# Performance work log

Hardware: AMD Instinct MI355X
Metric: run time of the kernel (lower is better)

## Reference

```python
import jax, jax.numpy as jnp
import numpy as np

D_MODEL = 2048
D_STATE = 16
D_CONV = 4
EXPAND = 2
D_INNER = EXPAND * D_MODEL  # 4096
DT_RANK = 128               # ceil(2048/16)
BATCH = 2
SEQ = 1024


def setup_inputs() -> dict:
    key = jax.random.key(0)
    ks = jax.random.split(key, 10)
    n = lambda k, shape, scale: jax.random.normal(k, shape, dtype=jnp.float32) * scale
    # A_log = log(arange(1..N)) broadcast over channels, exactly as in the torch init
    A_log = jnp.log(jnp.tile(jnp.arange(1, D_STATE + 1, dtype=jnp.float32)[None, :], (D_INNER, 1)))
    return {
        "hidden_states": n(ks[0], (BATCH, SEQ, D_MODEL), 1.0),
        "W_in": n(ks[1], (2 * D_INNER, D_MODEL), 0.02),
        "conv_w": n(ks[2], (D_INNER, D_CONV), 0.2),
        "conv_b": n(ks[3], (D_INNER,), 0.02),
        "W_x": n(ks[4], (DT_RANK + 2 * D_STATE, D_INNER), 0.02),
        "W_dt": n(ks[5], (D_INNER, DT_RANK), 0.05),
        "b_dt": n(ks[6], (D_INNER,), 0.5) - 4.0,  # softplus(b_dt) ~ small dt, like inv-softplus init
        "A_log": A_log,
        "D_skip": jnp.ones((D_INNER,), jnp.float32),
        "W_out": n(ks[7], (D_MODEL, D_INNER), 0.02),
    }


def _mamba_forward(hidden_states, W_in, conv_w, conv_b, W_x, W_dt, b_dt, A_log, D_skip, W_out):
    B, L, _ = hidden_states.shape
    # in_proj then split into x (SSM path) and z (gate)
    xz = hidden_states @ W_in.T                      # (B, L, 2*Di)
    x, z = jnp.split(xz, 2, axis=-1)                 # (B, L, Di) each
    # causal depthwise conv1d (kernel D_CONV, left pad D_CONV-1) + SiLU
    xp = jnp.pad(x, ((0, 0), (D_CONV - 1, 0), (0, 0)))
    xc = conv_b
    for k in range(D_CONV):
        xc = xc + conv_w[:, k] * xp[:, k:k + L, :]
    x = jax.nn.silu(xc)                              # (B, L, Di)
    # input-dependent dt, B, C
    x_dbl = x @ W_x.T                                # (B, L, dt_rank + 2N)
    dt_low, B_in, C_in = jnp.split(x_dbl, [DT_RANK, DT_RANK + D_STATE], axis=-1)
    dt = dt_low @ W_dt.T                             # (B, L, Di); bias added inside scan (delta_bias)
    delta = jax.nn.softplus(dt + b_dt)               # (B, L, Di)
    A = -jnp.exp(A_log)                              # (Di, N)

    def step(h, inp):
        delta_t, u_t, B_t, C_t = inp                 # (B,Di),(B,Di),(B,N),(B,N)
        dA = jnp.exp(delta_t[..., None] * A)         # (B, Di, N)
        h = dA * h + (delta_t * u_t)[..., None] * B_t[:, None, :]
        y_t = jnp.einsum('bdn,bn->bd', h, C_t)
        return h, y_t

    h0 = jnp.zeros((B, D_INNER, D_STATE), x.dtype)
    xs = (jnp.swapaxes(delta, 0, 1), jnp.swapaxes(x, 0, 1),
          jnp.swapaxes(B_in, 0, 1), jnp.swapaxes(C_in, 0, 1))
    _, ys = jax.lax.scan(step, h0, xs)               # ys: (L, B, Di)
    y = jnp.swapaxes(ys, 0, 1)                       # (B, L, Di)
    y = y + D_skip * x                               # skip connection
    y = y * jax.nn.silu(z)                           # output gating
    return y @ W_out.T                               # (B, L, D_MODEL)


def reference(hidden_states, W_in, conv_w, conv_b, W_x, W_dt, b_dt, A_log, D_skip, W_out):
    return _mamba_forward(hidden_states, W_in, conv_w, conv_b, W_x, W_dt, b_dt, A_log, D_skip, W_out)
```

## Files before the change

### kernel.cpp

```cpp
#include <hip/hip_runtime.h>
#include <hip/hip_bf16.h>


#define BATCH 2
#define SEQ 1024
#define DMODEL 2048
#define DINNER 4096
#define DSTATE 16
#define DTRANK 128
#define ROWS (BATCH * SEQ)
#define XDBL_N (DTRANK + 2 * DSTATE)
#define NCHUNK 32
#define LOG2_NCHUNK 5
#define CLEN (SEQ / NCHUNK)
#define WXPAD 192
#define SPLITK 16

typedef unsigned short ushort_t;
typedef __attribute__((ext_vector_type(8))) short short8;
typedef __attribute__((ext_vector_type(4))) float f32x4;

__device__ __forceinline__ ushort_t bf16_rne(float f) {
  unsigned u = __float_as_uint(f);
  return (ushort_t)((u + 0x7FFFu + ((u >> 16) & 1u)) >> 16);
}

__global__ __launch_bounds__(256) void cast_bf16(
    const float* __restrict__ x, ushort_t* __restrict__ o, int n4) {
  int i = blockIdx.x * 256 + threadIdx.x;
  if (i >= n4) return;
  float4 v = ((const float4*)x)[i];
  ushort4 h;
  h.x = bf16_rne(v.x); h.y = bf16_rne(v.y);
  h.z = bf16_rne(v.z); h.w = bf16_rne(v.w);
  ((ushort4*)o)[i] = h;
}

__global__ __launch_bounds__(256) void cast_wx(
    const float* __restrict__ wx, ushort_t* __restrict__ o) {
  int i = blockIdx.x * 256 + threadIdx.x;
  if (i >= WXPAD * (DINNER / 4)) return;
  int row = i >> 10;
  ushort4 h = {0, 0, 0, 0};
  if (row < XDBL_N) {
    float4 v = ((const float4*)wx)[i];
    h.x = bf16_rne(v.x); h.y = bf16_rne(v.y);
    h.z = bf16_rne(v.z); h.w = bf16_rne(v.w);
  }
  ((ushort4*)o)[i] = h;
}

template <int TM, int TN, int EPI, bool SK, bool SWZ>
__global__ __launch_bounds__(256, 2) void gemm_bf16(
    const ushort_t* __restrict__ X, int lda,
    const ushort_t* __restrict__ W, int ldb,
    const float* __restrict__ bias,
    float* __restrict__ C, int ldc, int kslice, size_t sstride) {
  constexpr int MI = TM / 32;
  constexpr int NI = TN / 32;
  constexpr int G = (TM + TN) / 32;
  __shared__ __attribute__((aligned(16))) ushort_t lds[(TM + TN) * 64];

  const int tid = threadIdx.x;
  const int lane = tid & 63;
  const int w = tid >> 6;
  const int wm = w & 1, wn = w >> 1;
  int bx = blockIdx.x, by = blockIdx.y;
  if (SWZ) {
    const int bid = by * 16 + bx;
    const int cpx = (16 * gridDim.y) >> 3;
    const int sz = (bid & 7) * cpx + (bid >> 3);
    bx = sz & 15;
    by = sz >> 4;
  }
  const int m0 = bx * TM;
  const int n0 = by * TN;
  const int kbase = SK ? blockIdx.z * kslice : 0;

  const int lrow = lane >> 3;
  const int csw = (lane & 7) ^ lrow;
  const int quad = lane >> 4;
  const int l15 = lane & 15;
  const int x0 = quad ^ (lane & 7);
  const int baseA = (wm * (TM / 2) + l15) * 64;
  const int baseB = (TM + wn * (TN / 2) + l15) * 64;

  f32x4 acc[MI][NI] = {};

  for (int kt = 0; kt < kslice; kt += 64) {
#pragma unroll
    for (int j = 0; j < G; j++) {
      const int r0 = (w * G + j) * 8;
      const int row = r0 + lrow;
      const ushort_t* src = (r0 < TM)
          ? X + (size_t)(m0 + row) * lda + kbase + kt + csw * 8
          : W + (size_t)(n0 + row - TM) * ldb + kbase + kt + csw * 8;
      __builtin_amdgcn_global_load_lds(
          (const __attribute__((address_space(1))) unsigned int*)src,
          (__attribute__((address_space(3))) unsigned int*)&lds[r0 * 64],
          16, 0, 0);
    }
    __syncthreads();

#pragma unroll
    for (int ks = 0; ks < 2; ks++) {
      const int xo = (x0 ^ (ks * 4)) * 8;
      short8 a[MI], b[NI];
#pragma unroll
      for (int mi = 0; mi < MI; mi++)
        a[mi] = *(const short8*)&lds[baseA + mi * 1024 + xo];
#pragma unroll
      for (int ni = 0; ni < NI; ni++)
        b[ni] = *(const short8*)&lds[baseB + ni * 1024 + xo];
#pragma unroll
      for (int mi = 0; mi < MI; mi++)
#pragma unroll
        for (int ni = 0; ni < NI; ni++)
          acc[mi][ni] = __builtin_amdgcn_mfma_f32_16x16x32_bf16(
              a[mi], b[ni], acc[mi][ni], 0, 0, 0);
    }
    __syncthreads();
  }

  float* Cs = SK ? (C + (size_t)blockIdx.z * sstride) : C;
#pragma unroll
  for (int mi = 0; mi < MI; mi++)
#pragma unroll
    for (int ni = 0; ni < NI; ni++) {
      int row = m0 + wm * (TM / 2) + mi * 16 + quad * 4;
      int col = n0 + wn * (TN / 2) + ni * 16 + l15;
#pragma unroll
      for (int r = 0; r < 4; r++) {
        float v = acc[mi][ni][r];
        if (EPI == 1) {
          v += bias[col];
          v = (v > 20.f) ? v : log1pf(__expf(v));
        }
        Cs[(size_t)(row + r) * ldc + col] = v;
      }
    }
}

__device__ __forceinline__ void bar() {
  asm volatile("" ::: "memory");
  __builtin_amdgcn_s_barrier();
  asm volatile("" ::: "memory");
}
#define VMWAIT(n) asm volatile("s_waitcnt vmcnt(" #n ")" ::: "memory")
#define LGKM0 asm volatile("s_waitcnt lgkmcnt(0)" ::: "memory")
#define SCHED0 __builtin_amdgcn_sched_barrier(0)

#define CLUSTER(AF, BF, MH, NH)                                           \
  do {                                                                    \
    __builtin_amdgcn_s_setprio(1);                                        \
    _Pragma("unroll")                                                     \
    for (int mi = 0; mi < 4; mi++)                                        \
      _Pragma("unroll")                                                   \
      for (int ni = 0; ni < 2; ni++)                                      \
        _Pragma("unroll")                                                 \
        for (int ks = 0; ks < 2; ks++)                                    \
          acc[(MH) * 4 + mi][(NH) * 2 + ni] =                             \
              __builtin_amdgcn_mfma_f32_16x16x32_bf16(                    \
                  AF[mi][ks], BF[ni][ks],                                 \
                  acc[(MH) * 4 + mi][(NH) * 2 + ni], 0, 0, 0);            \
    __builtin_amdgcn_s_setprio(0);                                        \
  } while (0)

__global__ __launch_bounds__(512, 2) void gemm256(
    const ushort_t* __restrict__ X, int lda,
    const ushort_t* __restrict__ W, int ldb,
    float* __restrict__ C, int ldc, int K) {
  __shared__ __attribute__((aligned(16))) ushort_t lds[65536];
  const int tid = threadIdx.x;
  const int lane = tid & 63;
  const int w = tid >> 6;
  const int wm = w >> 2, wn = w & 3;
  const int bid = blockIdx.y * 8 + blockIdx.x;
  const int swz = (bid & 7) * 32 + (bid >> 3);
  const int m0 = (swz & 7) * 256;
  const int n0 = (swz >> 3) * 256;
  const int lrow = lane >> 3;
  const int csw = (lane & 7) ^ lrow;
  const int quad = lane >> 4;
  const int l15 = lane & 15;
  const int sx = lane & 7;

  f32x4 acc[8][4] = {};
  short8 a[4][2], b0[2][2], b1[2][2];

  const ushort_t* Asrc = X + (size_t)(m0 + w * 8 + lrow) * lda + csw * 8;
  const ushort_t* Bsrc = W + (size_t)(n0 + w * 8 + lrow) * ldb + csw * 8;

  auto stA = [&](int buf, int g, int kt) {
    __builtin_amdgcn_global_load_lds(
        (const __attribute__((address_space(1))) unsigned int*)
            (Asrc + (size_t)g * 64 * lda + kt),
        (__attribute__((address_space(3))) unsigned int*)
            &lds[buf * 16384 + (g * 64 + w * 8) * 64],
        16, 0, 0);
  };
  auto stB = [&](int buf, int g, int kt) {
    __builtin_amdgcn_global_load_lds(
        (const __attribute__((address_space(1))) unsigned int*)
            (Bsrc + (size_t)g * 64 * ldb + kt),
        (__attribute__((address_space(3))) unsigned int*)
            &lds[32768 + buf * 16384 + (g * 64 + w * 8) * 64],
        16, 0, 0);
  };
  auto rdA = [&](int buf, int half, int mi, int ks) {
    int row = wm * 128 + half * 64 + mi * 16 + l15;
    int ch = (ks * 4 + quad) ^ sx;
    return *(const short8*)&lds[buf * 16384 + row * 64 + ch * 8];
  };
  auto rdB = [&](int buf, int nh, int ni, int ks) {
    int row = wn * 64 + nh * 32 + ni * 16 + l15;
    int ch = (ks * 4 + quad) ^ sx;
    return *(const short8*)&lds[32768 + buf * 16384 + row * 64 + ch * 8];
  };

#pragma unroll
  for (int g = 0; g < 4; g++) stA(0, g, 0);
#pragma unroll
  for (int g = 0; g < 4; g++) stB(0, g, 0);
  VMWAIT(0);
  bar();

  const int NT = K / 64;
  int cur = 0;
  for (int t = 0; t < NT - 1; ++t) {
    const int nxt = cur ^ 1;
    const int k2 = (t + 1) * 64;
#pragma unroll
    for (int mi = 0; mi < 4; mi++)
#pragma unroll
      for (int ks = 0; ks < 2; ks++) a[mi][ks] = rdA(cur, 0, mi, ks);
#pragma unroll
    for (int ni = 0; ni < 2; ni++)
#pragma unroll
      for (int ks = 0; ks < 2; ks++) b0[ni][ks] = rdB(cur, 0, ni, ks);
    stB(nxt, 0, k2); stB(nxt, 1, k2); stA(nxt, 0, k2); stA(nxt, 2, k2);
    bar();
    LGKM0; SCHED0;
    CLUSTER(a, b0, 0, 0);
    bar();
#pragma unroll
    for (int ni = 0; ni < 2; ni++)
#pragma unroll
      for (int ks = 0; ks < 2; ks++) b1[ni][ks] = rdB(cur, 1, ni, ks);
    stB(nxt, 2, k2); stB(nxt, 3, k2); stA(nxt, 1, k2); stA(nxt, 3, k2);
    bar();
    LGKM0; SCHED0;
    CLUSTER(a, b1, 0, 1);
    VMWAIT(8);
    bar();
#pragma unroll
    for (int mi = 0; mi < 4; mi++)
#pragma unroll
      for (int ks = 0; ks < 2; ks++) a[mi][ks] = rdA(cur, 1, mi, ks);
    bar();
    LGKM0; SCHED0;
    CLUSTER(a, b1, 1, 1);
    bar();
    CLUSTER(a, b0, 1, 0);
    VMWAIT(2);
    bar();
    cur = nxt;
  }
  {
#pragma unroll
    for (int mi = 0; mi < 4; mi++)
#pragma unroll
      for (int ks = 0; ks < 2; ks++) a[mi][ks] = rdA(cur, 0, mi, ks);
#pragma unroll
    for (int ni = 0; ni < 2; ni++)
#pragma unroll
      for (int ks = 0; ks < 2; ks++) b0[ni][ks] = rdB(cur, 0, ni, ks);
    bar();
    LGKM0; SCHED0;
    CLUSTER(a, b0, 0, 0);
    bar();
#pragma unroll
    for (int ni = 0; ni < 2; ni++)
#pragma unroll
      for (int ks = 0; ks < 2; ks++) b1[ni][ks] = rdB(cur, 1, ni, ks);
    bar();
    LGKM0; SCHED0;
    CLUSTER(a, b1, 0, 1);
    VMWAIT(0);
    bar();
#pragma unroll
    for (int mi = 0; mi < 4; mi++)
#pragma unroll
      for (int ks = 0; ks < 2; ks++) a[mi][ks] = rdA(cur, 1, mi, ks);
    bar();
    LGKM0; SCHED0;
    CLUSTER(a, b1, 1, 1);
    CLUSTER(a, b0, 1, 0);
  }

#pragma unroll
  for (int mi = 0; mi < 8; mi++)
#pragma unroll
    for (int ni = 0; ni < 4; ni++) {
      int row = m0 + wm * 128 + mi * 16 + quad * 4;
      int col = n0 + wn * 64 + ni * 16 + l15;
#pragma unroll
      for (int r = 0; r < 4; r++)
        C[(size_t)(row + r) * ldc + col] = acc[mi][ni][r];
    }
}

__global__ __launch_bounds__(192) void reduce_sk(
    const float* __restrict__ partials, float* __restrict__ xdbl,
    ushort_t* __restrict__ dtb) {
  int m = blockIdx.x;
  int c = threadIdx.x;
  if (c >= XDBL_N) return;
  float s = 0.f;
#pragma unroll
  for (int z = 0; z < SPLITK; z++)
    s += partials[(size_t)z * ROWS * WXPAD + (size_t)m * WXPAD + c];
  xdbl[(size_t)m * XDBL_N + c] = s;
  if (c < DTRANK) dtb[(size_t)m * DTRANK + c] = bf16_rne(s);
}

__global__ __launch_bounds__(256) void conv_silu(
    const float* __restrict__ xz, const float* __restrict__ cw,
    const float* __restrict__ cb, float* __restrict__ xs,
    ushort_t* __restrict__ xsb) {
  int idx = blockIdx.x * 256 + threadIdx.x;
  if (idx >= ROWS * DINNER / 4) return;
  int d4 = idx & (DINNER / 4 - 1);
  int bt = idx >> 10;
  int t = bt & (SEQ - 1);
  int d = d4 * 4;
  float4 c4 = *(const float4*)&cb[d];
  float wv[4][4];
  *(float4*)wv[0] = *(const float4*)&cw[(d + 0) * 4];
  *(float4*)wv[1] = *(const float4*)&cw[(d + 1) * 4];
  *(float4*)wv[2] = *(const float4*)&cw[(d + 2) * 4];
  *(float4*)wv[3] = *(const float4*)&cw[(d + 3) * 4];
  float a0 = c4.x, a1 = c4.y, a2 = c4.z, a3 = c4.w;
#pragma unroll
  for (int k = 0; k < 4; k++) {
    int tt = t - 3 + k;
    if (tt >= 0) {
      float4 v = *(const float4*)&xz[(size_t)(bt - 3 + k) * (2 * DINNER) + d];
      a0 += wv[0][k] * v.x;
      a1 += wv[1][k] * v.y;
      a2 += wv[2][k] * v.z;
      a3 += wv[3][k] * v.w;
    }
  }
  float4 s;
  s.x = a0 / (1.f + __expf(-a0));
  s.y = a1 / (1.f + __expf(-a1));
  s.z = a2 / (1.f + __expf(-a2));
  s.w = a3 / (1.f + __expf(-a3));
  *(float4*)&xs[(size_t)bt * DINNER + d] = s;
  ushort4 h;
  h.x = bf16_rne(s.x); h.y = bf16_rne(s.y);
  h.z = bf16_rne(s.z); h.w = bf16_rne(s.w);
  *(ushort4*)&xsb[(size_t)bt * DINNER + d] = h;
}

__global__ __launch_bounds__(256) void scan_pass1(
    const float* __restrict__ delta, const float* __restrict__ xs,
    const float* __restrict__ xdbl, const float* __restrict__ A_log,
    float* __restrict__ hpart, float* __restrict__ sumd) {
  int g = blockIdx.x * 256 + threadIdx.x;
  int d = g & (DINNER - 1);
  int rest = g >> 12;
  int c = rest & (NCHUNK - 1);
  int b = rest >> LOG2_NCHUNK;

  float Adn[16];
#pragma unroll
  for (int q = 0; q < 4; q++) {
    float4 a = *(const float4*)&A_log[d * 16 + q * 4];
    Adn[q * 4 + 0] = -__expf(a.x); Adn[q * 4 + 1] = -__expf(a.y);
    Adn[q * 4 + 2] = -__expf(a.z); Adn[q * 4 + 3] = -__expf(a.w);
  }

  float h[16] = {};
  float sd = 0.f;
  const size_t t0 = (size_t)b * SEQ + c * CLEN;
  const float* dp = delta + t0 * DINNER + d;
  const float* up = xs + t0 * DINNER + d;
  const float* xb = xdbl + t0 * XDBL_N + DTRANK;

  for (int i = 0; i < CLEN; i++) {
    float dt = dp[(size_t)i * DINNER];
    float u = up[(size_t)i * DINNER];
    sd += dt;
    float du = dt * u;
    float Bv[16];
#pragma unroll
    for (int q = 0; q < 4; q++)
      *(float4*)&Bv[q * 4] = *(const float4*)&xb[i * XDBL_N + q * 4];
#pragma unroll
    for (int n = 0; n < 16; n++)
      h[n] = __expf(dt * Adn[n]) * h[n] + du * Bv[n];
  }

  float* hp = hpart + ((size_t)(c * BATCH + b) * DINNER + d) * 16;
#pragma unroll
  for (int q = 0; q < 4; q++) *(float4*)&hp[q * 4] = *(const float4*)&h[q * 4];
  sumd[(size_t)(c * BATCH + b) * DINNER + d] = sd;
}

__global__ __launch_bounds__(256) void scan_pass2(
    float* __restrict__ hph, const float* __restrict__ sumd,
    const float* __restrict__ A_log) {
  int g = blockIdx.x * 256 + threadIdx.x;
  int n = g & 15;
  int d = (g >> 4) & (DINNER - 1);
  int b = g >> 16;

  float Adn = -__expf(A_log[d * 16 + n]);
  float h = 0.f;
  for (int c = 0; c < NCHUNK; c++) {
    size_t base = (size_t)(c * BATCH + b) * DINNER + d;
    float part = hph[base * 16 + n];
    hph[base * 16 + n] = h;
    h = __expf(Adn * sumd[base]) * h + part;
  }
}

__global__ __launch_bounds__(256) void scan_pass3(
    const float* __restrict__ xz, const float* __restrict__ xs,
    const float* __restrict__ xdbl, const float* __restrict__ A_log,
    const float* __restrict__ D_skip, const float* __restrict__ h0,
    const float* __restrict__ delta, ushort_t* __restrict__ gated) {
  int g = blockIdx.x * 256 + threadIdx.x;
  int d = g & (DINNER - 1);
  int rest = g >> 12;
  int c = rest & (NCHUNK - 1);
  int b = rest >> LOG2_NCHUNK;

  float Adn[16];
#pragma unroll
  for (int q = 0; q < 4; q++) {
    float4 a = *(const float4*)&A_log[d * 16 + q * 4];
    Adn[q * 4 + 0] = -__expf(a.x); Adn[q * 4 + 1] = -__expf(a.y);
    Adn[q * 4 + 2] = -__expf(a.z); Adn[q * 4 + 3] = -__expf(a.w);
  }
  float Dd = D_skip[d];

  float h[16];
  const float* hp = h0 + ((size_t)(c * BATCH + b) * DINNER + d) * 16;
#pragma unroll
  for (int q = 0; q < 4; q++) *(float4*)&h[q * 4] = *(const float4*)&hp[q * 4];

  const size_t t0 = (size_t)b * SEQ + c * CLEN;
  const float* dl = delta + t0 * DINNER + d;
  const float* up = xs + t0 * DINNER + d;
  const float* zb = xz + t0 * (2 * DINNER) + DINNER + d;
  const float* xb = xdbl + t0 * XDBL_N + DTRANK;
  ushort_t* gp = gated + t0 * DINNER + d;

  for (int i = 0; i < CLEN; i++) {
    float dt = dl[(size_t)i * DINNER];
    float u = up[(size_t)i * DINNER];
    float du = dt * u;
    float Bv[16], Cv[16];
#pragma unroll
    for (int q = 0; q < 4; q++) {
      *(float4*)&Bv[q * 4] = *(const float4*)&xb[i * XDBL_N + q * 4];
      *(float4*)&Cv[q * 4] = *(const float4*)&xb[i * XDBL_N + DSTATE + q * 4];
    }
    float y = 0.f;
#pragma unroll
    for (int n = 0; n < 16; n++) {
      h[n] = __expf(dt * Adn[n]) * h[n] + du * Bv[n];
      y += h[n] * Cv[n];
    }
    float z = zb[(size_t)i * (2 * DINNER)];
    float sz = z / (1.f + __expf(-z));
    gp[(size_t)i * DINNER] = bf16_rne((y + Dd * u) * sz);
  }
}

extern "C" void kernel_launch(void* const* d_in, const int* in_sizes, int n_in,
                              void* d_out, int out_size, void* d_ws, size_t ws_size,
                              hipStream_t stream) {
  const float* hidden = (const float*)d_in[0];
  const float* W_in   = (const float*)d_in[1];
  const float* conv_w = (const float*)d_in[2];
  const float* conv_b = (const float*)d_in[3];
  const float* W_x    = (const float*)d_in[4];
  const float* W_dt   = (const float*)d_in[5];
  const float* b_dt   = (const float*)d_in[6];
  const float* A_log  = (const float*)d_in[7];
  const float* D_skip = (const float*)d_in[8];
  const float* W_out  = (const float*)d_in[9];
  float* out = (float*)d_out;

  float* ws    = (float*)d_ws;
  float* xz    = ws;
  float* xs    = xz + (size_t)ROWS * 2 * DINNER;
  float* xdbl  = xs + (size_t)ROWS * DINNER;
  float* delta = xdbl + (size_t)ROWS * XDBL_N;
  float* sumd  = delta + (size_t)ROWS * DINNER;
  float* hph   = sumd + (size_t)BATCH * DINNER * NCHUNK;
  ushort_t* Hb   = (ushort_t*)(hph + (size_t)BATCH * DINNER * NCHUNK * DSTATE);
  ushort_t* Wb1  = Hb + (size_t)ROWS * DMODEL;
  ushort_t* Wxb  = Wb1 + (size_t)2 * DINNER * DMODEL;
  ushort_t* Wdtb = Wxb + (size_t)WXPAD * DINNER;
  ushort_t* xsb  = Wdtb + (size_t)DINNER * DTRANK;
  ushort_t* dtb  = xsb + (size_t)ROWS * DINNER;
  float* partials = (float*)Wb1;
  ushort_t* Woutb = Wb1;
  ushort_t* gatedb = Wb1 + (size_t)DMODEL * DINNER;

  dim3 blk(256);

  cast_bf16<<<(ROWS * DMODEL / 4 + 255) / 256, blk, 0, stream>>>(
      hidden, Hb, ROWS * DMODEL / 4);
  cast_bf16<<<(2 * DINNER * DMODEL / 4 + 255) / 256, blk, 0, stream>>>(
      W_in, Wb1, 2 * DINNER * DMODEL / 4);

  gemm256<<<dim3(8, 32), dim3(512), 0, stream>>>(
      Hb, DMODEL, Wb1, DMODEL, xz, 2 * DINNER, DMODEL);

  conv_silu<<<(ROWS * DINNER / 4 + 255) / 256, blk, 0, stream>>>(
      xz, conv_w, conv_b, xs, xsb);

  cast_wx<<<(WXPAD * DINNER / 4 + 255) / 256, blk, 0, stream>>>(W_x, Wxb);
  cast_bf16<<<(DINNER * DTRANK / 4 + 255) / 256, blk, 0, stream>>>(
      W_dt, Wdtb, DINNER * DTRANK / 4);

  gemm_bf16<128, 64, 0, true, false><<<dim3(16, 3, SPLITK), blk, 0, stream>>>(
      xsb, DINNER, Wxb, DINNER, nullptr, partials, WXPAD, DINNER / SPLITK,
      (size_t)ROWS * WXPAD);
  reduce_sk<<<ROWS, dim3(WXPAD), 0, stream>>>(partials, xdbl, dtb);

  gemm_bf16<128, 128, 1, false, true><<<dim3(16, 32), blk, 0, stream>>>(
      dtb, DTRANK, Wdtb, DTRANK, b_dt, delta, DINNER, DTRANK, 0);

  scan_pass1<<<(BATCH * DINNER * NCHUNK) / 256, blk, 0, stream>>>(
      delta, xs, xdbl, A_log, hph, sumd);
  scan_pass2<<<(BATCH * DINNER * DSTATE) / 256, blk, 0, stream>>>(
      hph, sumd, A_log);
  scan_pass3<<<(BATCH * DINNER * NCHUNK) / 256, blk, 0, stream>>>(
      xz, xs, xdbl, A_log, D_skip, hph, delta, gatedb);

  cast_bf16<<<(DMODEL * DINNER / 4 + 255) / 256, blk, 0, stream>>>(
      W_out, Woutb, DMODEL * DINNER / 4);

  gemm_bf16<128, 64, 0, false, true><<<dim3(16, 32), blk, 0, stream>>>(
      gatedb, DINNER, Woutb, DINNER, nullptr, out, DMODEL, DINNER, 0);
}
```

Before: 457.7 us.

## Restructure 256x256 GEMM pipeline into 8-phase half-tile prefetch with remapped B layout

Rewrites the gemm256 main loop to process two K-tiles per iteration in eight phases. Each global-to-LDS load group is issued into a buffer half as soon as that half has been consumed, and the prologue preloads part of the second buffer. The per-wave B column mapping changes so each wave's two N-halves sit 128 columns apart, with matching epilogue indexing, presumably to reduce LDS bank conflicts. The goal is tighter overlap of global loads with MFMA clusters. It relies on fine-grained vmcnt/lgkmcnt waits, and a mistake in their ordering could race on LDS.

```diff
diff --git a/kernel.cpp b/kernel.cpp
--- a/kernel.cpp
+++ b/kernel.cpp
@@ -148,6 +148,7 @@
 }
 #define VMWAIT(n) asm volatile("s_waitcnt vmcnt(" #n ")" ::: "memory")
 #define LGKM0 asm volatile("s_waitcnt lgkmcnt(0)" ::: "memory")
+#define LGKM8 asm volatile("s_waitcnt lgkmcnt(8)" ::: "memory")
 #define SCHED0 __builtin_amdgcn_sched_barrier(0)
 
 #define CLUSTER(AF, BF, MH, NH)                                           \
@@ -165,6 +166,18 @@
                   acc[(MH) * 4 + mi][(NH) * 2 + ni], 0, 0, 0);            \
     __builtin_amdgcn_s_setprio(0);                                        \
   } while (0)
+
+#define RD_A(buf, half)                                                   \
+  _Pragma("unroll")                                                       \
+  for (int mi = 0; mi < 4; mi++)                                          \
+    _Pragma("unroll")                                                     \
+    for (int ks = 0; ks < 2; ks++) a[mi][ks] = rdA(buf, half, mi, ks)
+
+#define RD_B(dst, buf, nh)                                                \
+  _Pragma("unroll")                                                       \
+  for (int ni = 0; ni < 2; ni++)                                          \
+    _Pragma("unroll")                                                     \
+    for (int ks = 0; ks < 2; ks++) dst[ni][ks] = rdB(buf, nh, ni, ks)
 
 __global__ __launch_bounds__(512, 2) void gemm256(
     const ushort_t* __restrict__ X, int lda,
@@ -213,7 +226,7 @@
     return *(const short8*)&lds[buf * 16384 + row * 64 + ch * 8];
   };
   auto rdB = [&](int buf, int nh, int ni, int ks) {
-    int row = wn * 64 + nh * 32 + ni * 16 + l15;
+    int row = nh * 128 + wn * 32 + ni * 16 + l15;
     int ch = (ks * 4 + quad) ^ sx;
     return *(const short8*)&lds[32768 + buf * 16384 + row * 64 + ch * 8];
   };
@@ -222,91 +235,104 @@
   for (int g = 0; g < 4; g++) stA(0, g, 0);
 #pragma unroll
   for (int g = 0; g < 4; g++) stB(0, g, 0);
+  stA(1, 0, 64); stA(1, 2, 64);
+  stB(1, 0, 64); stB(1, 1, 64);
+  stB(1, 2, 64); stB(1, 3, 64);
   VMWAIT(0);
   bar();
 
-  const int NT = K / 64;
-  int cur = 0;
-  for (int t = 0; t < NT - 1; ++t) {
-    const int nxt = cur ^ 1;
-    const int k2 = (t + 1) * 64;
-#pragma unroll
-    for (int mi = 0; mi < 4; mi++)
-#pragma unroll
-      for (int ks = 0; ks < 2; ks++) a[mi][ks] = rdA(cur, 0, mi, ks);
-#pragma unroll
-    for (int ni = 0; ni < 2; ni++)
-#pragma unroll
-      for (int ks = 0; ks < 2; ks++) b0[ni][ks] = rdB(cur, 0, ni, ks);
-    stB(nxt, 0, k2); stB(nxt, 1, k2); stA(nxt, 0, k2); stA(nxt, 2, k2);
-    bar();
-    LGKM0; SCHED0;
+  const int NI = K / 128;
+  for (int i = 0; i < NI - 1; ++i) {
+    const int k1 = (2 * i + 1) * 64;
+    const int ks0 = (2 * i + 2) * 64;
+    const int ks1 = (2 * i + 3) * 64;
+    RD_A(0, 0); RD_B(b0, 0, 0);
+    stA(1, 1, k1); stA(1, 3, k1);
+    LGKM8;
+    bar(); LGKM0; SCHED0;
     CLUSTER(a, b0, 0, 0);
     bar();
-#pragma unroll
-    for (int ni = 0; ni < 2; ni++)
-#pragma unroll
-      for (int ks = 0; ks < 2; ks++) b1[ni][ks] = rdB(cur, 1, ni, ks);
-    stB(nxt, 2, k2); stB(nxt, 3, k2); stA(nxt, 1, k2); stA(nxt, 3, k2);
-    bar();
-    LGKM0; SCHED0;
+    RD_B(b1, 0, 1);
+    stA(0, 0, ks0); stA(0, 2, ks0);
+    bar(); LGKM0; SCHED0;
     CLUSTER(a, b1, 0, 1);
-    VMWAIT(8);
-    bar();
-#pragma unroll
-    for (int mi = 0; mi < 4; mi++)
-#pragma unroll
-      for (int ks = 0; ks < 2; ks++) a[mi][ks] = rdA(cur, 1, mi, ks);
-    bar();
-    LGKM0; SCHED0;
+    bar();
+    RD_A(0, 1);
+    stB(0, 0, ks0); stB(0, 1, ks0);
+    bar(); LGKM0; SCHED0;
     CLUSTER(a, b1, 1, 1);
     bar();
+    stB(0, 2, ks0); stB(0, 3, ks0);
+    bar(); SCHED0;
     CLUSTER(a, b0, 1, 0);
-    VMWAIT(2);
-    bar();
-    cur = nxt;
+    VMWAIT(6);
+    bar();
+    RD_A(1, 0); RD_B(b0, 1, 0);
+    stA(0, 1, ks0); stA(0, 3, ks0);
+    LGKM8;
+    bar(); LGKM0; SCHED0;
+    CLUSTER(a, b0, 0, 0);
+    bar();
+    RD_B(b1, 1, 1);
+    stA(1, 0, ks1); stA(1, 2, ks1);
+    bar(); LGKM0; SCHED0;
+    CLUSTER(a, b1, 0, 1);
+    bar();
+    RD_A(1, 1);
+    stB(1, 0, ks1); stB(1, 1, ks1);
+    bar(); LGKM0; SCHED0;
+    CLUSTER(a, b1, 1, 1);
+    bar();
+    stB(1, 2, ks1); stB(1, 3, ks1);
+    bar(); SCHED0;
+    CLUSTER(a, b0, 1, 0);
+    VMWAIT(6);
+    bar();
   }
   {
-#pragma unroll
-    for (int mi = 0; mi < 4; mi++)
-#pragma unroll
-      for (int ks = 0; ks < 2; ks++) a[mi][ks] = rdA(cur, 0, mi, ks);
-#pragma unroll
-    for (int ni = 0; ni < 2; ni++)
-#pragma unroll
-      for (int ks = 0; ks < 2; ks++) b0[ni][ks] = rdB(cur, 0, ni, ks);
-    bar();
-    LGKM0; SCHED0;
+    const int k1 = (K / 64 - 1) * 64;
+    RD_A(0, 0); RD_B(b0, 0, 0);
+    stA(1, 1, k1); stA(1, 3, k1);
+    LGKM8;
+    bar(); LGKM0; SCHED0;
     CLUSTER(a, b0, 0, 0);
     bar();
-#pragma unroll
-    for (int ni = 0; ni < 2; ni++)
-#pragma unroll
-      for (int ks = 0; ks < 2; ks++) b1[ni][ks] = rdB(cur, 1, ni, ks);
-    bar();
-    LGKM0; SCHED0;
+    RD_B(b1, 0, 1);
+    bar(); LGKM0; SCHED0;
     CLUSTER(a, b1, 0, 1);
+    bar();
+    RD_A(0, 1);
+    bar(); LGKM0; SCHED0;
+    CLUSTER(a, b1, 1, 1);
+    bar();
+    SCHED0;
+    CLUSTER(a, b0, 1, 0);
     VMWAIT(0);
     bar();
-#pragma unroll
-    for (int mi = 0; mi < 4; mi++)
-#pragma unroll
-      for (int ks = 0; ks < 2; ks++) a[mi][ks] = rdA(cur, 1, mi, ks);
-    bar();
-    LGKM0; SCHED0;
+    RD_A(1, 0); RD_B(b0, 1, 0);
+    LGKM8;
+    bar(); LGKM0; SCHED0;
+    CLUSTER(a, b0, 0, 0);
+    bar();
+    RD_B(b1, 1, 1);
+    bar(); LGKM0; SCHED0;
+    CLUSTER(a, b1, 0, 1);
+    bar();
+    RD_A(1, 1);
+    bar(); LGKM0; SCHED0;
     CLUSTER(a, b1, 1, 1);
     CLUSTER(a, b0, 1, 0);
   }
 
 #pragma unroll
-  for (int mi = 0; mi < 8; mi++)
-#pragma unroll
-    for (int ni = 0; ni < 4; ni++) {
-      int row = m0 + wm * 128 + mi * 16 + quad * 4;
-      int col = n0 + wn * 64 + ni * 16 + l15;
+  for (int mj = 0; mj < 8; mj++)
+#pragma unroll
+    for (int nj = 0; nj < 4; nj++) {
+      int row = m0 + wm * 128 + mj * 16 + quad * 4;
+      int col = n0 + (nj >> 1) * 128 + wn * 32 + (nj & 1) * 16 + l15;
 #pragma unroll
       for (int r = 0; r < 4; r++)
-        C[(size_t)(row + r) * ldc + col] = acc[mi][ni][r];
+        C[(size_t)(row + r) * ldc + col] = acc[mj][nj][r];
     }
 }
 
```

Result: no change. 451.0 us (-1.5%).
